# Kernel tuning notes

Hardware: AMD Instinct MI355X
Metric: run time of the kernel (lower is better)

The kernel has to match this reference:

```python
import jax, jax.numpy as jnp
import numpy as np

SRC_DIM = 64
DEST_DIM = 64
EDGE_DIM = 16
HID = 128
NHEAD = 4
B, S_CNT, D_CNT, K = 16, 1000, 1000, 32


def setup_inputs() -> dict:
    key = jax.random.key(0)
    ks = jax.random.split(key, 14)
    N = B * D_CNT
    sc = 0.05
    src = jax.random.normal(ks[0], (B, S_CNT, SRC_DIM), jnp.float32)
    dest = jax.random.normal(ks[1], (B, D_CNT, DEST_DIM), jnp.float32)
    # index 0 points at the prepended zero-padding row; valid ids in [0, B*S_CNT]
    adj = jax.random.randint(ks[2], (K, N), 0, B * S_CNT + 1, jnp.int32)
    mask = jax.random.randint(ks[3], (N, K), 0, 2) > 0
    mask = mask.at[:, 0].set(False)  # guarantee >=1 unmasked key per query
    edges = jax.random.normal(ks[4], (K, N, EDGE_DIM), jnp.float32)
    W_src = jax.random.normal(ks[5], (HID, SRC_DIM + EDGE_DIM), jnp.float32) * sc
    b_src = jnp.zeros((HID,), jnp.float32)
    W_dest = jax.random.normal(ks[6], (HID, DEST_DIM), jnp.float32) * sc
    b_dest = jnp.zeros((HID,), jnp.float32)
    in_proj_w = jax.random.normal(ks[7], (3 * HID, HID), jnp.float32) * sc
    in_proj_b = jax.random.normal(ks[8], (3 * HID,), jnp.float32) * sc
    out_proj_w = jax.random.normal(ks[9], (HID, HID), jnp.float32) * sc
    out_proj_b = jnp.zeros((HID,), jnp.float32)
    ln_g = jnp.ones((HID,), jnp.float32)
    ln_b = jnp.zeros((HID,), jnp.float32)
    return {"src": src, "dest": dest, "adj": adj, "mask": mask, "edges": edges,
            "W_src": W_src, "b_src": b_src, "W_dest": W_dest, "b_dest": b_dest,
            "in_proj_w": in_proj_w, "in_proj_b": in_proj_b,
            "out_proj_w": out_proj_w, "out_proj_b": out_proj_b,
            "ln_g": ln_g, "ln_b": ln_b}


def reference(src, dest, adj, mask, edges, W_src, b_src, W_dest, b_dest,
              in_proj_w, in_proj_b, out_proj_w, out_proj_b, ln_g, ln_b):
    B_, S_, Ds = src.shape
    _, Dn, Dd = dest.shape
    Kn = adj.shape[0]
    N = B_ * Dn
    H = W_src.shape[0]
    nh = NHEAD
    hd = H // nh
    # gather neighbor features, row 0 = zero padding
    src_flat = jnp.concatenate([jnp.zeros((1, Ds), src.dtype), src.reshape(-1, Ds)], 0)
    gathered = src_flat[adj.reshape(-1)].reshape(Kn, N, Ds)
    x = jnp.concatenate([gathered, edges], axis=-1)          # (K, N, Ds+E)
    src_in = jax.nn.gelu(x @ W_src.T + b_src, approximate=False)       # (K, N, H)
    dest_in = jax.nn.gelu(dest.reshape(N, Dd) @ W_dest.T + b_dest, approximate=False)  # (N, H)
    Wq, Wk, Wv = jnp.split(in_proj_w, 3, axis=0)
    bq, bk, bv = jnp.split(in_proj_b, 3, axis=0)
    q = ((dest_in @ Wq.T + bq).reshape(N, nh, hd)) * (1.0 / np.sqrt(hd))
    k = (src_in @ Wk.T + bk).reshape(Kn, N, nh, hd)
    v = (src_in @ Wv.T + bv).reshape(Kn, N, nh, hd)
    scores = jnp.einsum('nhd,knhd->nhk', q, k)               # (N, nh, K)
    scores = jnp.where(mask[:, None, :], -jnp.inf, scores)
    attn = jax.nn.softmax(scores, axis=-1)
    ctx = jnp.einsum('nhk,knhd->nhd', attn, v).reshape(N, H)
    out = ctx @ out_proj_w.T + out_proj_b
    out = out * 2.0  # dest_emb + dropout(dest_emb), dropout identity in eval
    mu = out.mean(-1, keepdims=True)
    var = ((out - mu) ** 2).mean(-1, keepdims=True)
    out = (out - mu) / jnp.sqrt(var + 1e-5) * ln_g + ln_b
    return out.reshape(B_, Dn, H)
```

## Files before the change

kernel.cpp:

```cpp
#include <hip/hip_runtime.h>
#include <hip/hip_bf16.h>
#include <math.h>

#define N_DEST 16000
#define KN     32
#define HIDN   128
#define NH     4
#define SRCD   64
#define EDGED  16
#define XD     80
#define XDP    96
#define WPB    4
#define NPW    2

#define WSB_OFF 0
#define WKV_OFF 12288
#define WDB_OFF 45056
#define WQB_OFF 53248
#define WOB_OFF 69632
#define PREP_TOT 86016

typedef __attribute__((ext_vector_type(8))) short frag8;
typedef __attribute__((ext_vector_type(4))) float f32x4;

__device__ __forceinline__ float gelu_tanh(float x) {
    float t = x * x;
    float m = fmaf(t, -0.07135481627f, -1.5957691216f);
    float e = __expf(x * m);
    return __fdividef(x, 1.0f + e);
}
__device__ __forceinline__ unsigned short f2bf(float f) {
    __hip_bfloat16 h = __float2bfloat16(f);
    union { __hip_bfloat16 h; unsigned short u; } c; c.h = h; return c.u;
}
__device__ __forceinline__ unsigned int pk2bf(float x, float y) {
    __hip_bfloat162 h2 = __float22bfloat162_rn(make_float2(x, y));
    union { __hip_bfloat162 h; unsigned int u; } c; c.h = h2; return c.u;
}
__device__ __forceinline__ float bflo(unsigned int u) {
    union { unsigned int u; float f; } c; c.u = u << 16; return c.f;
}
__device__ __forceinline__ float bfhi(unsigned int u) {
    union { unsigned int u; float f; } c; c.u = u & 0xFFFF0000u; return c.f;
}
__device__ __forceinline__ float dot8(uint4 w, float4 x0, float4 x1, float acc) {
    acc = fmaf(bflo(w.x), x0.x, acc); acc = fmaf(bfhi(w.x), x0.y, acc);
    acc = fmaf(bflo(w.y), x0.z, acc); acc = fmaf(bfhi(w.y), x0.w, acc);
    acc = fmaf(bflo(w.z), x1.x, acc); acc = fmaf(bfhi(w.z), x1.y, acc);
    acc = fmaf(bflo(w.w), x1.z, acc); acc = fmaf(bfhi(w.w), x1.w, acc);
    return acc;
}
__device__ __forceinline__ frag8 pack_frag(float4 f0, float4 f1) {
    union { frag8 f; uint4 u; } c;
    c.u.x = pk2bf(f0.x, f0.y); c.u.y = pk2bf(f0.z, f0.w);
    c.u.z = pk2bf(f1.x, f1.y); c.u.w = pk2bf(f1.z, f1.w);
    return c.f;
}
__device__ __forceinline__ frag8 zero_frag() {
    union { frag8 f; uint4 u; } c;
    c.u = make_uint4(0u, 0u, 0u, 0u);
    return c.f;
}

__global__ void prep_weights(const float* __restrict__ W_src,
                             const float* __restrict__ W_dest,
                             const float* __restrict__ Wqkv,
                             const float* __restrict__ Wo,
                             unsigned short* __restrict__ ws) {
    int i = blockIdx.x * 256 + threadIdx.x;
    if (i < WKV_OFF) {
        int r = i / XDP, c = i - r * XDP;
        ws[i] = f2bf(c < XD ? W_src[r * XD + c] : 0.0f);
    } else if (i < WDB_OFF) {
        int j = i - WKV_OFF;
        ws[i] = f2bf(Wqkv[128 * HIDN + j]);
    } else if (i < WQB_OFF) {
        ws[i] = f2bf(W_dest[i - WDB_OFF]);
    } else if (i < WOB_OFF) {
        ws[i] = f2bf(Wqkv[i - WQB_OFF]);
    } else if (i < PREP_TOT) {
        ws[i] = f2bf(Wo[i - WOB_OFF]);
    }
}

__device__ __forceinline__ void gemm_d_node(
    int n, int a0, int a1,
    const float* __restrict__ src, const float* __restrict__ edges,
    const float* __restrict__ b_src, const unsigned short* __restrict__ Wsb,
    unsigned short (*sinp)[128], int lg, int lm)
{
    frag8 aall[3][2];
    #pragma unroll
    for (int kt = 0; kt < 2; ++kt) {
        const int c0 = kt * 32 + lg * 8;
        if (a0) {
            const float4* p = (const float4*)(src + (size_t)(a0 - 1) * SRCD + c0);
            aall[kt][0] = pack_frag(p[0], p[1]);
        } else aall[kt][0] = zero_frag();
        if (a1) {
            const float4* p = (const float4*)(src + (size_t)(a1 - 1) * SRCD + c0);
            aall[kt][1] = pack_frag(p[0], p[1]);
        } else aall[kt][1] = zero_frag();
    }
    if (lg < 2) {
        const float4* p0 = (const float4*)(edges + ((size_t)lm * N_DEST + n) * EDGED + lg * 8);
        const float4* p1 = (const float4*)(edges + ((size_t)(lm + 16) * N_DEST + n) * EDGED + lg * 8);
        aall[2][0] = pack_frag(p0[0], p0[1]);
        aall[2][1] = pack_frag(p1[0], p1[1]);
    } else {
        aall[2][0] = zero_frag(); aall[2][1] = zero_frag();
    }

    #pragma unroll 1
    for (int half = 0; half < 2; ++half) {
        f32x4 acc[2][4];
        #pragma unroll
        for (int ct = 0; ct < 4; ++ct) {
            float bias = b_src[(half * 4 + ct) * 16 + lm];
            acc[0][ct] = (f32x4){bias, bias, bias, bias};
            acc[1][ct] = (f32x4){bias, bias, bias, bias};
        }
        #pragma unroll
        for (int kt = 0; kt < 3; ++kt) {
            #pragma unroll
            for (int ct = 0; ct < 4; ++ct) {
                frag8 b = *(const frag8*)(Wsb + (size_t)((half * 4 + ct) * 16 + lm) * XDP + kt * 32 + lg * 8);
                acc[0][ct] = __builtin_amdgcn_mfma_f32_16x16x32_bf16(aall[kt][0], b, acc[0][ct], 0, 0, 0);
                acc[1][ct] = __builtin_amdgcn_mfma_f32_16x16x32_bf16(aall[kt][1], b, acc[1][ct], 0, 0, 0);
            }
        }
        #pragma unroll
        for (int r = 0; r < 2; ++r)
            #pragma unroll
            for (int ct = 0; ct < 4; ++ct)
                #pragma unroll
                for (int e = 0; e < 4; ++e) {
                    const int row = r * 16 + lg * 4 + e;
                    const int cb  = ((half * 4 + ct) * 16 + lm) * 2;
                    const int byt = (cb ^ ((row & 7) << 4));
                    *(unsigned short*)((char*)&sinp[row][0] + byt) =
                        f2bf(gelu_tanh(acc[r][ct][e]));
                }
    }
}

__device__ __forceinline__ void softmax_head(
    const f32x4 (&acc)[2][4], unsigned mw, const float* __restrict__ sq,
    float* __restrict__ attn_row, int ch, int hp, int lg, int lm)
{
    float q0 = sq[ch * 64 + hp * 32 + lm];
    float q1 = sq[ch * 64 + hp * 32 + 16 + lm];
    float vals[8];
    #pragma unroll
    for (int r = 0; r < 2; ++r)
        #pragma unroll
        for (int e = 0; e < 4; ++e) {
            float v = acc[r][2 * hp][e] * q0 + acc[r][2 * hp + 1][e] * q1;
            v += __shfl_xor(v, 1); v += __shfl_xor(v, 2);
            v += __shfl_xor(v, 4); v += __shfl_xor(v, 8);
            vals[r * 4 + e] = v;
        }
    float m8 = -1e30f;
    #pragma unroll
    for (int j = 0; j < 8; ++j) {
        const int kk = (j >> 2) * 16 + lg * 4 + (j & 3);
        if ((mw >> kk) & 1u) vals[j] = -1e30f;
        m8 = fmaxf(m8, vals[j]);
    }
    m8 = fmaxf(m8, __shfl_xor(m8, 16));
    m8 = fmaxf(m8, __shfl_xor(m8, 32));
    float ex[8], s8 = 0.0f;
    #pragma unroll
    for (int j = 0; j < 8; ++j) { ex[j] = __expf(vals[j] - m8); s8 += ex[j]; }
    s8 += __shfl_xor(s8, 16); s8 += __shfl_xor(s8, 32);
    const float inv = __fdividef(1.0f, s8);
    if (lm == 0) {
        *(float4*)&attn_row[lg * 4] =
            make_float4(ex[0] * inv, ex[1] * inv, ex[2] * inv, ex[3] * inv);
        *(float4*)&attn_row[16 + lg * 4] =
            make_float4(ex[4] * inv, ex[5] * inv, ex[6] * inv, ex[7] * inv);
    }
}

__device__ __forceinline__ void pv_node(
    const f32x4 (&acc)[2][4], const float (*attn)[KN],
    float* __restrict__ ctx, int ch, int lg, int lm)
{
    const int hb = (ch - 2) * 2;
    float4 at[2][2];
    #pragma unroll
    for (int hp = 0; hp < 2; ++hp)
        #pragma unroll
        for (int r = 0; r < 2; ++r)
            at[hp][r] = *(const float4*)&attn[hb + hp][r * 16 + lg * 4];
    #pragma unroll
    for (int ct = 0; ct < 4; ++ct) {
        const int hp = ct >> 1;
        float v = 0.0f;
        #pragma unroll
        for (int r = 0; r < 2; ++r) {
            v = fmaf(at[hp][r].x, acc[r][ct][0], v);
            v = fmaf(at[hp][r].y, acc[r][ct][1], v);
            v = fmaf(at[hp][r].z, acc[r][ct][2], v);
            v = fmaf(at[hp][r].w, acc[r][ct][3], v);
        }
        v += __shfl_xor(v, 16); v += __shfl_xor(v, 32);
        if (lg == 0) ctx[(ch - 2) * 64 + ct * 16 + lm] = v;
    }
}

__global__ __launch_bounds__(256, 2) void fused_gat_wave(
    const float* __restrict__ src,
    const float* __restrict__ dest,
    const int*   __restrict__ adj,
    const int*   __restrict__ mask,
    const float* __restrict__ edges,
    const float* __restrict__ b_src,
    const float* __restrict__ b_dest,
    const float* __restrict__ bqkv,
    const float* __restrict__ bo,
    const float* __restrict__ ln_g,
    const float* __restrict__ ln_b,
    const unsigned short* __restrict__ ws,
    float* __restrict__ out)
{
    const int tid  = threadIdx.x;
    const int wv   = tid >> 6;
    const int lane = tid & 63;
    const int lg   = lane >> 4;
    const int lm   = lane & 15;
    const int n0   = (blockIdx.x * WPB + wv) * NPW;

    const unsigned short* Wsb = ws + WSB_OFF;
    const unsigned short* Wkv = ws + WKV_OFF;
    const unsigned short* Wdb = ws + WDB_OFF;
    const unsigned short* Wqb = ws + WQB_OFF;
    const unsigned short* Wob = ws + WOB_OFF;

    __shared__ __align__(16) unsigned short s_sin[WPB][NPW][KN][128];
    __shared__ __align__(16) float s_dc[WPB][NPW][HIDN];
    __shared__ __align__(16) float s_q[WPB][NPW][HIDN];
    __shared__ __align__(16) float s_attn[WPB][NPW][NH][KN];

    const int a00 = adj[lm * N_DEST + n0];
    const int a01 = adj[(lm + 16) * N_DEST + n0];
    const int a10 = adj[lm * N_DEST + n0 + 1];
    const int a11 = adj[(lm + 16) * N_DEST + n0 + 1];
    const int mv = mask[n0 * KN + lane];
    const unsigned long long bal = __ballot(mv != 0);
    const unsigned mw0 = (unsigned)bal;
    const unsigned mw1 = (unsigned)(bal >> 32);

    {
        const float* dr0 = dest + (size_t)n0 * SRCD;
        const float* dr1 = dest + (size_t)(n0 + 1) * SRCD;
        float bd0 = b_dest[lane], bd1 = b_dest[lane + 64];
        float da0 = bd0, da1 = bd1, db0 = bd0, db1 = bd1;
        #pragma unroll
        for (int c = 0; c < 8; ++c) {
            float4 xa0 = *(const float4*)(dr0 + c * 8);
            float4 xa1 = *(const float4*)(dr0 + c * 8 + 4);
            float4 xb0 = *(const float4*)(dr1 + c * 8);
            float4 xb1 = *(const float4*)(dr1 + c * 8 + 4);
            uint4 w0 = *(const uint4*)(Wdb + (size_t)lane * SRCD + c * 8);
            uint4 w1 = *(const uint4*)(Wdb + (size_t)(lane + 64) * SRCD + c * 8);
            da0 = dot8(w0, xa0, xa1, da0); da1 = dot8(w1, xa0, xa1, da1);
            db0 = dot8(w0, xb0, xb1, db0); db1 = dot8(w1, xb0, xb1, db1);
        }
        s_dc[wv][0][lane]      = gelu_tanh(da0);
        s_dc[wv][0][lane + 64] = gelu_tanh(da1);
        s_dc[wv][1][lane]      = gelu_tanh(db0);
        s_dc[wv][1][lane + 64] = gelu_tanh(db1);
    }
    __builtin_amdgcn_wave_barrier();

    {
        float bq0 = bqkv[lane], bq1 = bqkv[lane + 64];
        float qa0 = bq0, qa1 = bq1, qb0 = bq0, qb1 = bq1;
        #pragma unroll
        for (int c = 0; c < 16; ++c) {
            float4 xa0 = *(const float4*)&s_dc[wv][0][c * 8];
            float4 xa1 = *(const float4*)&s_dc[wv][0][c * 8 + 4];
            float4 xb0 = *(const float4*)&s_dc[wv][1][c * 8];
            float4 xb1 = *(const float4*)&s_dc[wv][1][c * 8 + 4];
            uint4 w0 = *(const uint4*)(Wqb + (size_t)lane * HIDN + c * 8);
            uint4 w1 = *(const uint4*)(Wqb + (size_t)(lane + 64) * HIDN + c * 8);
            qa0 = dot8(w0, xa0, xa1, qa0); qa1 = dot8(w1, xa0, xa1, qa1);
            qb0 = dot8(w0, xb0, xb1, qb0); qb1 = dot8(w1, xb0, xb1, qb1);
        }
        const float sc = 0.17677669529663688110f;
        s_q[wv][0][lane]      = qa0 * sc;
        s_q[wv][0][lane + 64] = qa1 * sc;
        s_q[wv][1][lane]      = qb0 * sc;
        s_q[wv][1][lane + 64] = qb1 * sc;
    }
    __builtin_amdgcn_wave_barrier();

    gemm_d_node(n0,     a00, a01, src, edges, b_src, Wsb, s_sin[wv][0], lg, lm);
    gemm_d_node(n0 + 1, a10, a11, src, edges, b_src, Wsb, s_sin[wv][1], lg, lm);
    __builtin_amdgcn_wave_barrier();

    #pragma unroll 1
    for (int ch = 0; ch < 4; ++ch) {
        f32x4 ac0[2][4], ac1[2][4];
        #pragma unroll
        for (int ct = 0; ct < 4; ++ct) {
            float bias = bqkv[128 + ch * 64 + ct * 16 + lm];
            ac0[0][ct] = (f32x4){bias, bias, bias, bias};
            ac0[1][ct] = ac0[0][ct];
            ac1[0][ct] = ac0[0][ct];
            ac1[1][ct] = ac0[0][ct];
        }
        #pragma unroll
        for (int kt = 0; kt < 4; ++kt) {
            const int off = (kt * 64 + lg * 16) ^ ((lm & 7) << 4);
            frag8 a00f = *(const frag8*)((const char*)&s_sin[wv][0][lm][0] + off);
            frag8 a01f = *(const frag8*)((const char*)&s_sin[wv][0][16 + lm][0] + off);
            frag8 a10f = *(const frag8*)((const char*)&s_sin[wv][1][lm][0] + off);
            frag8 a11f = *(const frag8*)((const char*)&s_sin[wv][1][16 + lm][0] + off);
            #pragma unroll
            for (int ct = 0; ct < 4; ++ct) {
                frag8 b = *(const frag8*)(Wkv + (size_t)(ch * 64 + ct * 16 + lm) * HIDN + kt * 32 + lg * 8);
                ac0[0][ct] = __builtin_amdgcn_mfma_f32_16x16x32_bf16(a00f, b, ac0[0][ct], 0, 0, 0);
                ac0[1][ct] = __builtin_amdgcn_mfma_f32_16x16x32_bf16(a01f, b, ac0[1][ct], 0, 0, 0);
                ac1[0][ct] = __builtin_amdgcn_mfma_f32_16x16x32_bf16(a10f, b, ac1[0][ct], 0, 0, 0);
                ac1[1][ct] = __builtin_amdgcn_mfma_f32_16x16x32_bf16(a11f, b, ac1[1][ct], 0, 0, 0);
            }
        }
        if (ch < 2) {
            #pragma unroll
            for (int hp = 0; hp < 2; ++hp) {
                const int head = ch * 2 + hp;
                softmax_head(ac0, mw0, s_q[wv][0], s_attn[wv][0][head], ch, hp, lg, lm);
                softmax_head(ac1, mw1, s_q[wv][1], s_attn[wv][1][head], ch, hp, lg, lm);
            }
        } else {
            pv_node(ac0, s_attn[wv][0], s_dc[wv][0], ch, lg, lm);
            pv_node(ac1, s_attn[wv][1], s_dc[wv][1], ch, lg, lm);
        }
    }
    __builtin_amdgcn_wave_barrier();

    {
        float bo0 = bo[lane], bo1 = bo[lane + 64];
        float oa0 = bo0, oa1 = bo1, ob0 = bo0, ob1 = bo1;
        #pragma unroll
        for (int c = 0; c < 16; ++c) {
            float4 xa0 = *(const float4*)&s_dc[wv][0][c * 8];
            float4 xa1 = *(const float4*)&s_dc[wv][0][c * 8 + 4];
            float4 xb0 = *(const float4*)&s_dc[wv][1][c * 8];
            float4 xb1 = *(const float4*)&s_dc[wv][1][c * 8 + 4];
            uint4 w0 = *(const uint4*)(Wob + (size_t)lane * HIDN + c * 8);
            uint4 w1 = *(const uint4*)(Wob + (size_t)(lane + 64) * HIDN + c * 8);
            oa0 = dot8(w0, xa0, xa1, oa0); oa1 = dot8(w1, xa0, xa1, oa1);
            ob0 = dot8(w0, xb0, xb1, ob0); ob1 = dot8(w1, xb0, xb1, ob1);
        }
        float o00 = oa0 * 2.0f, o01 = oa1 * 2.0f;
        float o10 = ob0 * 2.0f, o11 = ob1 * 2.0f;
        float s0 = o00 + o01, ss0 = o00 * o00 + o01 * o01;
        float s1 = o10 + o11, ss1 = o10 * o10 + o11 * o11;
        #pragma unroll
        for (int off = 1; off < 64; off <<= 1) {
            s0  += __shfl_xor(s0, off);  ss0 += __shfl_xor(ss0, off);
            s1  += __shfl_xor(s1, off);  ss1 += __shfl_xor(ss1, off);
        }
        float mu0  = s0 * (1.0f / HIDN);
        float var0 = ss0 * (1.0f / HIDN) - mu0 * mu0;
        float rs0  = rsqrtf(var0 + 1e-5f);
        float mu1  = s1 * (1.0f / HIDN);
        float var1 = ss1 * (1.0f / HIDN) - mu1 * mu1;
        float rs1  = rsqrtf(var1 + 1e-5f);
        float g0 = ln_g[lane], g1 = ln_g[lane + 64];
        float t0 = ln_b[lane], t1 = ln_b[lane + 64];
        out[(size_t)n0 * HIDN + lane]            = (o00 - mu0) * rs0 * g0 + t0;
        out[(size_t)n0 * HIDN + lane + 64]       = (o01 - mu0) * rs0 * g1 + t1;
        out[(size_t)(n0 + 1) * HIDN + lane]      = (o10 - mu1) * rs1 * g0 + t0;
        out[(size_t)(n0 + 1) * HIDN + lane + 64] = (o11 - mu1) * rs1 * g1 + t1;
    }
}

extern "C" void kernel_launch(void* const* d_in, const int* in_sizes, int n_in,
                              void* d_out, int out_size, void* d_ws, size_t ws_size,
                              hipStream_t stream) {
    const float* src    = (const float*)d_in[0];
    const float* dest   = (const float*)d_in[1];
    const int*   adj    = (const int*)  d_in[2];
    const int*   mask   = (const int*)  d_in[3];
    const float* edges  = (const float*)d_in[4];
    const float* W_src  = (const float*)d_in[5];
    const float* b_src  = (const float*)d_in[6];
    const float* W_dest = (const float*)d_in[7];
    const float* b_dest = (const float*)d_in[8];
    const float* Wqkv   = (const float*)d_in[9];
    const float* bqkv   = (const float*)d_in[10];
    const float* Wo     = (const float*)d_in[11];
    const float* bo     = (const float*)d_in[12];
    const float* ln_g   = (const float*)d_in[13];
    const float* ln_b   = (const float*)d_in[14];
    float* outp = (float*)d_out;

    unsigned short* ws = (unsigned short*)d_ws;
    prep_weights<<<PREP_TOT / 256, 256, 0, stream>>>(W_src, W_dest, Wqkv, Wo, ws);

    fused_gat_wave<<<N_DEST / (WPB * NPW), 256, 0, stream>>>(
        src, dest, adj, mask, edges, b_src, b_dest, bqkv, bo, ln_g, ln_b,
        ws, outp);
}
```

Before: 334.7 us.

## Split fused GAT kernel into source-projection and attention kernels via global buffer

```diff
diff --git a/kernel.cpp b/kernel.cpp
--- a/kernel.cpp
+++ b/kernel.cpp
@@ -19,6 +19,9 @@
 #define WQB_OFF 53248
 #define WOB_OFF 69632
 #define PREP_TOT 86016
+#define SIN_OFF  PREP_TOT
+#define SIN_ELEMS ((size_t)N_DEST * KN * HIDN)
+#define WS_NEED_BYTES ((size_t)2 * (PREP_TOT + SIN_ELEMS))
 
 typedef __attribute__((ext_vector_type(8))) short frag8;
 typedef __attribute__((ext_vector_type(4))) float f32x4;
@@ -83,6 +86,308 @@
     }
 }
 
+__device__ __forceinline__ void softmax_head(
+    const f32x4 (&acc)[2][4], unsigned mw, const float* __restrict__ sq,
+    float* __restrict__ attn_row, int ch, int hp, int lg, int lm)
+{
+    float q0 = sq[ch * 64 + hp * 32 + lm];
+    float q1 = sq[ch * 64 + hp * 32 + 16 + lm];
+    float vals[8];
+    #pragma unroll
+    for (int r = 0; r < 2; ++r)
+        #pragma unroll
+        for (int e = 0; e < 4; ++e) {
+            float v = acc[r][2 * hp][e] * q0 + acc[r][2 * hp + 1][e] * q1;
+            v += __shfl_xor(v, 1); v += __shfl_xor(v, 2);
+            v += __shfl_xor(v, 4); v += __shfl_xor(v, 8);
+            vals[r * 4 + e] = v;
+        }
+    float m8 = -1e30f;
+    #pragma unroll
+    for (int j = 0; j < 8; ++j) {
+        const int kk = (j >> 2) * 16 + lg * 4 + (j & 3);
+        if ((mw >> kk) & 1u) vals[j] = -1e30f;
+        m8 = fmaxf(m8, vals[j]);
+    }
+    m8 = fmaxf(m8, __shfl_xor(m8, 16));
+    m8 = fmaxf(m8, __shfl_xor(m8, 32));
+    float ex[8], s8 = 0.0f;
+    #pragma unroll
+    for (int j = 0; j < 8; ++j) { ex[j] = __expf(vals[j] - m8); s8 += ex[j]; }
+    s8 += __shfl_xor(s8, 16); s8 += __shfl_xor(s8, 32);
+    const float inv = __fdividef(1.0f, s8);
+    if (lm == 0) {
+        *(float4*)&attn_row[lg * 4] =
+            make_float4(ex[0] * inv, ex[1] * inv, ex[2] * inv, ex[3] * inv);
+        *(float4*)&attn_row[16 + lg * 4] =
+            make_float4(ex[4] * inv, ex[5] * inv, ex[6] * inv, ex[7] * inv);
+    }
+}
+
+__device__ __forceinline__ void pv_node(
+    const f32x4 (&acc)[2][4], const float (*attn)[KN],
+    float* __restrict__ ctx, int ch, int lg, int lm)
+{
+    const int hb = (ch - 2) * 2;
+    float4 at[2][2];
+    #pragma unroll
+    for (int hp = 0; hp < 2; ++hp)
+        #pragma unroll
+        for (int r = 0; r < 2; ++r)
+            at[hp][r] = *(const float4*)&attn[hb + hp][r * 16 + lg * 4];
+    #pragma unroll
+    for (int ct = 0; ct < 4; ++ct) {
+        const int hp = ct >> 1;
+        float v = 0.0f;
+        #pragma unroll
+        for (int r = 0; r < 2; ++r) {
+            v = fmaf(at[hp][r].x, acc[r][ct][0], v);
+            v = fmaf(at[hp][r].y, acc[r][ct][1], v);
+            v = fmaf(at[hp][r].z, acc[r][ct][2], v);
+            v = fmaf(at[hp][r].w, acc[r][ct][3], v);
+        }
+        v += __shfl_xor(v, 16); v += __shfl_xor(v, 32);
+        if (lg == 0) ctx[(ch - 2) * 64 + ct * 16 + lm] = v;
+    }
+}
+
+__device__ __forceinline__ void gemm_d_node_g(
+    int n, int a0, int a1,
+    const float* __restrict__ src, const float* __restrict__ edges,
+    const float* __restrict__ b_src, const unsigned short* __restrict__ Wsb,
+    unsigned short* __restrict__ sinG, int lg, int lm)
+{
+    frag8 aall[3][2];
+    #pragma unroll
+    for (int kt = 0; kt < 2; ++kt) {
+        const int c0 = kt * 32 + lg * 8;
+        if (a0) {
+            const float4* p = (const float4*)(src + (size_t)(a0 - 1) * SRCD + c0);
+            aall[kt][0] = pack_frag(p[0], p[1]);
+        } else aall[kt][0] = zero_frag();
+        if (a1) {
+            const float4* p = (const float4*)(src + (size_t)(a1 - 1) * SRCD + c0);
+            aall[kt][1] = pack_frag(p[0], p[1]);
+        } else aall[kt][1] = zero_frag();
+    }
+    if (lg < 2) {
+        const float4* p0 = (const float4*)(edges + ((size_t)lm * N_DEST + n) * EDGED + lg * 8);
+        const float4* p1 = (const float4*)(edges + ((size_t)(lm + 16) * N_DEST + n) * EDGED + lg * 8);
+        aall[2][0] = pack_frag(p0[0], p0[1]);
+        aall[2][1] = pack_frag(p1[0], p1[1]);
+    } else {
+        aall[2][0] = zero_frag(); aall[2][1] = zero_frag();
+    }
+
+    unsigned short* sb = sinG + (size_t)n * KN * HIDN;
+    #pragma unroll 1
+    for (int half = 0; half < 2; ++half) {
+        f32x4 acc[2][4];
+        #pragma unroll
+        for (int ct = 0; ct < 4; ++ct) {
+            float bias = b_src[(half * 4 + ct) * 16 + lm];
+            acc[0][ct] = (f32x4){bias, bias, bias, bias};
+            acc[1][ct] = (f32x4){bias, bias, bias, bias};
+        }
+        #pragma unroll
+        for (int kt = 0; kt < 3; ++kt) {
+            #pragma unroll
+            for (int ct = 0; ct < 4; ++ct) {
+                frag8 b = *(const frag8*)(Wsb + (size_t)((half * 4 + ct) * 16 + lm) * XDP + kt * 32 + lg * 8);
+                acc[0][ct] = __builtin_amdgcn_mfma_f32_16x16x32_bf16(aall[kt][0], b, acc[0][ct], 0, 0, 0);
+                acc[1][ct] = __builtin_amdgcn_mfma_f32_16x16x32_bf16(aall[kt][1], b, acc[1][ct], 0, 0, 0);
+            }
+        }
+        #pragma unroll
+        for (int r = 0; r < 2; ++r)
+            #pragma unroll
+            for (int ct = 0; ct < 4; ++ct)
+                #pragma unroll
+                for (int e = 0; e < 4; ++e) {
+                    const int row = r * 16 + lg * 4 + e;
+                    const int col = (half * 4 + ct) * 16 + lm;
+                    sb[(size_t)row * HIDN + col] = f2bf(gelu_tanh(acc[r][ct][e]));
+                }
+    }
+}
+
+__global__ __launch_bounds__(256, 4) void gemm_d_all(
+    const float* __restrict__ src, const float* __restrict__ edges,
+    const int* __restrict__ adj, const float* __restrict__ b_src,
+    const unsigned short* __restrict__ ws, unsigned short* __restrict__ sinG)
+{
+    const int tid  = threadIdx.x;
+    const int wv   = tid >> 6;
+    const int lane = tid & 63;
+    const int lg   = lane >> 4;
+    const int lm   = lane & 15;
+    const int n0   = (blockIdx.x * WPB + wv) * NPW;
+    const unsigned short* Wsb = ws + WSB_OFF;
+
+    const int a00 = adj[lm * N_DEST + n0];
+    const int a01 = adj[(lm + 16) * N_DEST + n0];
+    const int a10 = adj[lm * N_DEST + n0 + 1];
+    const int a11 = adj[(lm + 16) * N_DEST + n0 + 1];
+
+    gemm_d_node_g(n0,     a00, a01, src, edges, b_src, Wsb, sinG, lg, lm);
+    gemm_d_node_g(n0 + 1, a10, a11, src, edges, b_src, Wsb, sinG, lg, lm);
+}
+
+__global__ __launch_bounds__(256, 4) void attn_all(
+    const float* __restrict__ dest,
+    const int*   __restrict__ mask,
+    const float* __restrict__ b_dest,
+    const float* __restrict__ bqkv,
+    const float* __restrict__ bo,
+    const float* __restrict__ ln_g,
+    const float* __restrict__ ln_b,
+    const unsigned short* __restrict__ ws,
+    const unsigned short* __restrict__ sinG,
+    float* __restrict__ out)
+{
+    const int tid  = threadIdx.x;
+    const int wv   = tid >> 6;
+    const int lane = tid & 63;
+    const int lg   = lane >> 4;
+    const int lm   = lane & 15;
+    const int n0   = (blockIdx.x * WPB + wv) * NPW;
+
+    const unsigned short* Wkv = ws + WKV_OFF;
+    const unsigned short* Wdb = ws + WDB_OFF;
+    const unsigned short* Wqb = ws + WQB_OFF;
+    const unsigned short* Wob = ws + WOB_OFF;
+
+    __shared__ __align__(16) float s_dc[WPB][NPW][HIDN];
+    __shared__ __align__(16) float s_q[WPB][NPW][HIDN];
+    __shared__ __align__(16) float s_attn[WPB][NPW][NH][KN];
+
+    const int mv = mask[n0 * KN + lane];
+    const unsigned long long bal = __ballot(mv != 0);
+    const unsigned mw0 = (unsigned)bal;
+    const unsigned mw1 = (unsigned)(bal >> 32);
+
+    {
+        const float* dr0 = dest + (size_t)n0 * SRCD;
+        const float* dr1 = dest + (size_t)(n0 + 1) * SRCD;
+        float bd0 = b_dest[lane], bd1 = b_dest[lane + 64];
+        float da0 = bd0, da1 = bd1, db0 = bd0, db1 = bd1;
+        #pragma unroll
+        for (int c = 0; c < 8; ++c) {
+            float4 xa0 = *(const float4*)(dr0 + c * 8);
+            float4 xa1 = *(const float4*)(dr0 + c * 8 + 4);
+            float4 xb0 = *(const float4*)(dr1 + c * 8);
+            float4 xb1 = *(const float4*)(dr1 + c * 8 + 4);
+            uint4 w0 = *(const uint4*)(Wdb + (size_t)lane * SRCD + c * 8);
+            uint4 w1 = *(const uint4*)(Wdb + (size_t)(lane + 64) * SRCD + c * 8);
+            da0 = dot8(w0, xa0, xa1, da0); da1 = dot8(w1, xa0, xa1, da1);
+            db0 = dot8(w0, xb0, xb1, db0); db1 = dot8(w1, xb0, xb1, db1);
+        }
+        s_dc[wv][0][lane]      = gelu_tanh(da0);
+        s_dc[wv][0][lane + 64] = gelu_tanh(da1);
+        s_dc[wv][1][lane]      = gelu_tanh(db0);
+        s_dc[wv][1][lane + 64] = gelu_tanh(db1);
+    }
+    __builtin_amdgcn_wave_barrier();
+
+    {
+        float bq0 = bqkv[lane], bq1 = bqkv[lane + 64];
+        float qa0 = bq0, qa1 = bq1, qb0 = bq0, qb1 = bq1;
+        #pragma unroll
+        for (int c = 0; c < 16; ++c) {
+            float4 xa0 = *(const float4*)&s_dc[wv][0][c * 8];
+            float4 xa1 = *(const float4*)&s_dc[wv][0][c * 8 + 4];
+            float4 xb0 = *(const float4*)&s_dc[wv][1][c * 8];
+            float4 xb1 = *(const float4*)&s_dc[wv][1][c * 8 + 4];
+            uint4 w0 = *(const uint4*)(Wqb + (size_t)lane * HIDN + c * 8);
+            uint4 w1 = *(const uint4*)(Wqb + (size_t)(lane + 64) * HIDN + c * 8);
+            qa0 = dot8(w0, xa0, xa1, qa0); qa1 = dot8(w1, xa0, xa1, qa1);
+            qb0 = dot8(w0, xb0, xb1, qb0); qb1 = dot8(w1, xb0, xb1, qb1);
+        }
+        const float sc = 0.17677669529663688110f;
+        s_q[wv][0][lane]      = qa0 * sc;
+        s_q[wv][0][lane + 64] = qa1 * sc;
+        s_q[wv][1][lane]      = qb0 * sc;
+        s_q[wv][1][lane + 64] = qb1 * sc;
+    }
+    __builtin_amdgcn_wave_barrier();
+
+    #pragma unroll 1
+    for (int nd = 0; nd < NPW; ++nd) {
+        const unsigned short* sb = sinG + (size_t)(n0 + nd) * KN * HIDN;
+        frag8 af0[4], af1[4];
+        #pragma unroll
+        for (int kt = 0; kt < 4; ++kt) {
+            af0[kt] = *(const frag8*)(sb + (size_t)lm * HIDN + kt * 32 + lg * 8);
+            af1[kt] = *(const frag8*)(sb + (size_t)(lm + 16) * HIDN + kt * 32 + lg * 8);
+        }
+        const unsigned mwn = nd ? mw1 : mw0;
+        #pragma unroll 1
+        for (int ch = 0; ch < 4; ++ch) {
+            f32x4 acc[2][4];
+            #pragma unroll
+            for (int ct = 0; ct < 4; ++ct) {
+                float bias = bqkv[128 + ch * 64 + ct * 16 + lm];
+                acc[0][ct] = (f32x4){bias, bias, bias, bias};
+                acc[1][ct] = acc[0][ct];
+            }
+            #pragma unroll
+            for (int kt = 0; kt < 4; ++kt) {
+                #pragma unroll
+                for (int ct = 0; ct < 4; ++ct) {
+                    frag8 b = *(const frag8*)(Wkv + (size_t)(ch * 64 + ct * 16 + lm) * HIDN + kt * 32 + lg * 8);
+                    acc[0][ct] = __builtin_amdgcn_mfma_f32_16x16x32_bf16(af0[kt], b, acc[0][ct], 0, 0, 0);
+                    acc[1][ct] = __builtin_amdgcn_mfma_f32_16x16x32_bf16(af1[kt], b, acc[1][ct], 0, 0, 0);
+                }
+            }
+            if (ch < 2) {
+                #pragma unroll
+                for (int hp = 0; hp < 2; ++hp)
+                    softmax_head(acc, mwn, s_q[wv][nd], s_attn[wv][nd][ch * 2 + hp], ch, hp, lg, lm);
+            } else {
+                pv_node(acc, s_attn[wv][nd], s_dc[wv][nd], ch, lg, lm);
+            }
+        }
+    }
+    __builtin_amdgcn_wave_barrier();
+
+    {
+        float bo0 = bo[lane], bo1 = bo[lane + 64];
+        float oa0 = bo0, oa1 = bo1, ob0 = bo0, ob1 = bo1;
+        #pragma unroll
+        for (int c = 0; c < 16; ++c) {
+            float4 xa0 = *(const float4*)&s_dc[wv][0][c * 8];
+            float4 xa1 = *(const float4*)&s_dc[wv][0][c * 8 + 4];
+            float4 xb0 = *(const float4*)&s_dc[wv][1][c * 8];
+            float4 xb1 = *(const float4*)&s_dc[wv][1][c * 8 + 4];
+            uint4 w0 = *(const uint4*)(Wob + (size_t)lane * HIDN + c * 8);
+            uint4 w1 = *(const uint4*)(Wob + (size_t)(lane + 64) * HIDN + c * 8);
+            oa0 = dot8(w0, xa0, xa1, oa0); oa1 = dot8(w1, xa0, xa1, oa1);
+            ob0 = dot8(w0, xb0, xb1, ob0); ob1 = dot8(w1, xb0, xb1, ob1);
+        }
+        float o00 = oa0 * 2.0f, o01 = oa1 * 2.0f;
+        float o10 = ob0 * 2.0f, o11 = ob1 * 2.0f;
+        float s0 = o00 + o01, ss0 = o00 * o00 + o01 * o01;
+        float s1 = o10 + o11, ss1 = o10 * o10 + o11 * o11;
+        #pragma unroll
+        for (int off = 1; off < 64; off <<= 1) {
+            s0  += __shfl_xor(s0, off);  ss0 += __shfl_xor(ss0, off);
+            s1  += __shfl_xor(s1, off);  ss1 += __shfl_xor(ss1, off);
+        }
+        float mu0  = s0 * (1.0f / HIDN);
+        float var0 = ss0 * (1.0f / HIDN) - mu0 * mu0;
+        float rs0  = rsqrtf(var0 + 1e-5f);
+        float mu1  = s1 * (1.0f / HIDN);
+        float var1 = ss1 * (1.0f / HIDN) - mu1 * mu1;
+        float rs1  = rsqrtf(var1 + 1e-5f);
+        float g0 = ln_g[lane], g1 = ln_g[lane + 64];
+        float t0 = ln_b[lane], t1 = ln_b[lane + 64];
+        out[(size_t)n0 * HIDN + lane]            = (o00 - mu0) * rs0 * g0 + t0;
+        out[(size_t)n0 * HIDN + lane + 64]       = (o01 - mu0) * rs0 * g1 + t1;
+        out[(size_t)(n0 + 1) * HIDN + lane]      = (o10 - mu1) * rs1 * g0 + t0;
+        out[(size_t)(n0 + 1) * HIDN + lane + 64] = (o11 - mu1) * rs1 * g1 + t1;
+    }
+}
+
 __device__ __forceinline__ void gemm_d_node(
     int n, int a0, int a1,
     const float* __restrict__ src, const float* __restrict__ edges,
@@ -144,84 +449,13 @@
     }
 }
 
-__device__ __forceinline__ void softmax_head(
-    const f32x4 (&acc)[2][4], unsigned mw, const float* __restrict__ sq,
-    float* __restrict__ attn_row, int ch, int hp, int lg, int lm)
-{
-    float q0 = sq[ch * 64 + hp * 32 + lm];
-    float q1 = sq[ch * 64 + hp * 32 + 16 + lm];
-    float vals[8];
-    #pragma unroll
-    for (int r = 0; r < 2; ++r)
-        #pragma unroll
-        for (int e = 0; e < 4; ++e) {
-            float v = acc[r][2 * hp][e] * q0 + acc[r][2 * hp + 1][e] * q1;
-            v += __shfl_xor(v, 1); v += __shfl_xor(v, 2);
-            v += __shfl_xor(v, 4); v += __shfl_xor(v, 8);
-            vals[r * 4 + e] = v;
-        }
-    float m8 = -1e30f;
-    #pragma unroll
-    for (int j = 0; j < 8; ++j) {
-        const int kk = (j >> 2) * 16 + lg * 4 + (j & 3);
-        if ((mw >> kk) & 1u) vals[j] = -1e30f;
-        m8 = fmaxf(m8, vals[j]);
-    }
-    m8 = fmaxf(m8, __shfl_xor(m8, 16));
-    m8 = fmaxf(m8, __shfl_xor(m8, 32));
-    float ex[8], s8 = 0.0f;
-    #pragma unroll
-    for (int j = 0; j < 8; ++j) { ex[j] = __expf(vals[j] - m8); s8 += ex[j]; }
-    s8 += __shfl_xor(s8, 16); s8 += __shfl_xor(s8, 32);
-    const float inv = __fdividef(1.0f, s8);
-    if (lm == 0) {
-        *(float4*)&attn_row[lg * 4] =
-            make_float4(ex[0] * inv, ex[1] * inv, ex[2] * inv, ex[3] * inv);
-        *(float4*)&attn_row[16 + lg * 4] =
-            make_float4(ex[4] * inv, ex[5] * inv, ex[6] * inv, ex[7] * inv);
-    }
-}
-
-__device__ __forceinline__ void pv_node(
-    const f32x4 (&acc)[2][4], const float (*attn)[KN],
-    float* __restrict__ ctx, int ch, int lg, int lm)
-{
-    const int hb = (ch - 2) * 2;
-    float4 at[2][2];
-    #pragma unroll
-    for (int hp = 0; hp < 2; ++hp)
-        #pragma unroll
-        for (int r = 0; r < 2; ++r)
-            at[hp][r] = *(const float4*)&attn[hb + hp][r * 16 + lg * 4];
-    #pragma unroll
-    for (int ct = 0; ct < 4; ++ct) {
-        const int hp = ct >> 1;
-        float v = 0.0f;
-        #pragma unroll
-        for (int r = 0; r < 2; ++r) {
-            v = fmaf(at[hp][r].x, acc[r][ct][0], v);
-            v = fmaf(at[hp][r].y, acc[r][ct][1], v);
-            v = fmaf(at[hp][r].z, acc[r][ct][2], v);
-            v = fmaf(at[hp][r].w, acc[r][ct][3], v);
-        }
-        v += __shfl_xor(v, 16); v += __shfl_xor(v, 32);
-        if (lg == 0) ctx[(ch - 2) * 64 + ct * 16 + lm] = v;
-    }
-}
-
-__global__ __launch_bounds__(256, 2) void fused_gat_wave(
-    const float* __restrict__ src,
-    const float* __restrict__ dest,
-    const int*   __restrict__ adj,
-    const int*   __restrict__ mask,
-    const float* __restrict__ edges,
-    const float* __restrict__ b_src,
-    const float* __restrict__ b_dest,
-    const float* __restrict__ bqkv,
-    const float* __restrict__ bo,
-    const float* __restrict__ ln_g,
-    const float* __restrict__ ln_b,
-    const unsigned short* __restrict__ ws,
+__global__ __launch_bounds__(256, 2) void fused_gat_fallback(
+    const float* __restrict__ src, const float* __restrict__ dest,
+    const int* __restrict__ adj, const int* __restrict__ mask,
+    const float* __restrict__ edges, const float* __restrict__ b_src,
+    const float* __restrict__ b_dest, const float* __restrict__ bqkv,
+    const float* __restrict__ bo, const float* __restrict__ ln_g,
+    const float* __restrict__ ln_b, const unsigned short* __restrict__ ws,
     float* __restrict__ out)
 {
     const int tid  = threadIdx.x;
@@ -273,7 +507,6 @@
         s_dc[wv][1][lane + 64] = gelu_tanh(db1);
     }
     __builtin_amdgcn_wave_barrier();
-
     {
         float bq0 = bqkv[lane], bq1 = bqkv[lane + 64];
         float qa0 = bq0, qa1 = bq1, qb0 = bq0, qb1 = bq1;
@@ -295,11 +528,9 @@
         s_q[wv][1][lane + 64] = qb1 * sc;
     }
     __builtin_amdgcn_wave_barrier();
-
     gemm_d_node(n0,     a00, a01, src, edges, b_src, Wsb, s_sin[wv][0], lg, lm);
     gemm_d_node(n0 + 1, a10, a11, src, edges, b_src, Wsb, s_sin[wv][1], lg, lm);
     __builtin_amdgcn_wave_barrier();
-
     #pragma unroll 1
     for (int ch = 0; ch < 4; ++ch) {
         f32x4 ac0[2][4], ac1[2][4];
@@ -340,7 +571,6 @@
         }
     }
     __builtin_amdgcn_wave_barrier();
-
     {
         float bo0 = bo[lane], bo1 = bo[lane + 64];
         float oa0 = bo0, oa1 = bo1, ob0 = bo0, ob1 = bo1;
@@ -402,7 +632,15 @@
     unsigned short* ws = (unsigned short*)d_ws;
     prep_weights<<<PREP_TOT / 256, 256, 0, stream>>>(W_src, W_dest, Wqkv, Wo, ws);
 
-    fused_gat_wave<<<N_DEST / (WPB * NPW), 256, 0, stream>>>(
-        src, dest, adj, mask, edges, b_src, b_dest, bqkv, bo, ln_g, ln_b,
-        ws, outp);
-}
+    if (ws_size >= WS_NEED_BYTES) {
+        unsigned short* sinG = ws + SIN_OFF;
+        gemm_d_all<<<N_DEST / (WPB * NPW), 256, 0, stream>>>(
+            src, edges, adj, b_src, ws, sinG);
+        attn_all<<<N_DEST / (WPB * NPW), 256, 0, stream>>>(
+            dest, mask, b_dest, bqkv, bo, ln_g, ln_b, ws, sinG, outp);
+    } else {
+        fused_gat_fallback<<<N_DEST / (WPB * NPW), 256, 0, stream>>>(
+            src, dest, adj, mask, edges, b_src, b_dest, bqkv, bo, ln_g, ln_b,
+            ws, outp);
+    }
+}
```

Result: slower. 390.1 us (+16.6%).

## Process four destination nodes per wave to amortize weight loads

Applied to the files above, without the earlier changes.

```diff
diff --git a/kernel.cpp b/kernel.cpp
--- a/kernel.cpp
+++ b/kernel.cpp
@@ -11,7 +11,7 @@
 #define XD     80
 #define XDP    96
 #define WPB    4
-#define NPW    2
+#define NPW    4
 
 #define WSB_OFF 0
 #define WKV_OFF 12288
@@ -43,11 +43,15 @@
 __device__ __forceinline__ float bfhi(unsigned int u) {
     union { unsigned int u; float f; } c; c.u = u & 0xFFFF0000u; return c.f;
 }
-__device__ __forceinline__ float dot8(uint4 w, float4 x0, float4 x1, float acc) {
-    acc = fmaf(bflo(w.x), x0.x, acc); acc = fmaf(bfhi(w.x), x0.y, acc);
-    acc = fmaf(bflo(w.y), x0.z, acc); acc = fmaf(bfhi(w.y), x0.w, acc);
-    acc = fmaf(bflo(w.z), x1.x, acc); acc = fmaf(bfhi(w.z), x1.y, acc);
-    acc = fmaf(bflo(w.w), x1.z, acc); acc = fmaf(bfhi(w.w), x1.w, acc);
+__device__ __forceinline__ void unpack8(uint4 w, float f[8]) {
+    f[0] = bflo(w.x); f[1] = bfhi(w.x); f[2] = bflo(w.y); f[3] = bfhi(w.y);
+    f[4] = bflo(w.z); f[5] = bfhi(w.z); f[6] = bflo(w.w); f[7] = bfhi(w.w);
+}
+__device__ __forceinline__ float dotu(const float f[8], float4 x0, float4 x1, float acc) {
+    acc = fmaf(f[0], x0.x, acc); acc = fmaf(f[1], x0.y, acc);
+    acc = fmaf(f[2], x0.z, acc); acc = fmaf(f[3], x0.w, acc);
+    acc = fmaf(f[4], x1.x, acc); acc = fmaf(f[5], x1.y, acc);
+    acc = fmaf(f[6], x1.z, acc); acc = fmaf(f[7], x1.w, acc);
     return acc;
 }
 __device__ __forceinline__ frag8 pack_frag(float4 f0, float4 f1) {
@@ -145,11 +149,9 @@
 }
 
 __device__ __forceinline__ void softmax_head(
-    const f32x4 (&acc)[2][4], unsigned mw, const float* __restrict__ sq,
-    float* __restrict__ attn_row, int ch, int hp, int lg, int lm)
+    const f32x4 (&acc)[2][4], unsigned mw, float q0, float q1,
+    float* __restrict__ attn_row, int hp, int lg, int lm)
 {
-    float q0 = sq[ch * 64 + hp * 32 + lm];
-    float q1 = sq[ch * 64 + hp * 32 + 16 + lm];
     float vals[8];
     #pragma unroll
     for (int r = 0; r < 2; ++r)
@@ -207,6 +209,70 @@
         v += __shfl_xor(v, 16); v += __shfl_xor(v, 32);
         if (lg == 0) ctx[(ch - 2) * 64 + ct * 16 + lm] = v;
     }
+}
+
+__device__ __forceinline__ void process_pair(
+    int na, int nb, int a0a, int a1a, int a0b, int a1b,
+    unsigned mwa, unsigned mwb,
+    float qla, float qha, float qlb, float qhb,
+    const float* __restrict__ src, const float* __restrict__ edges,
+    const float* __restrict__ b_src, const float* __restrict__ bqkv,
+    const unsigned short* __restrict__ Wsb, const unsigned short* __restrict__ Wkv,
+    unsigned short (*sinA)[128], unsigned short (*sinB)[128],
+    float* __restrict__ dcA, float* __restrict__ dcB,
+    float (*attnA)[KN], float (*attnB)[KN],
+    int lg, int lm)
+{
+    gemm_d_node(na, a0a, a1a, src, edges, b_src, Wsb, sinA, lg, lm);
+    gemm_d_node(nb, a0b, a1b, src, edges, b_src, Wsb, sinB, lg, lm);
+    __builtin_amdgcn_wave_barrier();
+
+    #pragma unroll 1
+    for (int ch = 0; ch < 4; ++ch) {
+        f32x4 ac0[2][4], ac1[2][4];
+        #pragma unroll
+        for (int ct = 0; ct < 4; ++ct) {
+            float bias = bqkv[128 + ch * 64 + ct * 16 + lm];
+            ac0[0][ct] = (f32x4){bias, bias, bias, bias};
+            ac0[1][ct] = ac0[0][ct];
+            ac1[0][ct] = ac0[0][ct];
+            ac1[1][ct] = ac0[0][ct];
+        }
+        #pragma unroll
+        for (int kt = 0; kt < 4; ++kt) {
+            const int off = (kt * 64 + lg * 16) ^ ((lm & 7) << 4);
+            frag8 a00f = *(const frag8*)((const char*)&sinA[lm][0] + off);
+            frag8 a01f = *(const frag8*)((const char*)&sinA[16 + lm][0] + off);
+            frag8 a10f = *(const frag8*)((const char*)&sinB[lm][0] + off);
+            frag8 a11f = *(const frag8*)((const char*)&sinB[16 + lm][0] + off);
+            #pragma unroll
+            for (int ct = 0; ct < 4; ++ct) {
+                frag8 b = *(const frag8*)(Wkv + (size_t)(ch * 64 + ct * 16 + lm) * HIDN + kt * 32 + lg * 8);
+                ac0[0][ct] = __builtin_amdgcn_mfma_f32_16x16x32_bf16(a00f, b, ac0[0][ct], 0, 0, 0);
+                ac0[1][ct] = __builtin_amdgcn_mfma_f32_16x16x32_bf16(a01f, b, ac0[1][ct], 0, 0, 0);
+                ac1[0][ct] = __builtin_amdgcn_mfma_f32_16x16x32_bf16(a10f, b, ac1[0][ct], 0, 0, 0);
+                ac1[1][ct] = __builtin_amdgcn_mfma_f32_16x16x32_bf16(a11f, b, ac1[1][ct], 0, 0, 0);
+            }
+        }
+        if (ch < 2) {
+            #pragma unroll
+            for (int hp = 0; hp < 2; ++hp) {
+                const int head = ch * 2 + hp;
+                float qsa = (ch == 0) ? qla : qha;
+                float qsb = (ch == 0) ? qlb : qhb;
+                float qa0 = __shfl(qsa, hp * 32 + lm);
+                float qa1 = __shfl(qsa, hp * 32 + 16 + lm);
+                float qb0 = __shfl(qsb, hp * 32 + lm);
+                float qb1 = __shfl(qsb, hp * 32 + 16 + lm);
+                softmax_head(ac0, mwa, qa0, qa1, attnA[head], hp, lg, lm);
+                softmax_head(ac1, mwb, qb0, qb1, attnB[head], hp, lg, lm);
+            }
+        } else {
+            pv_node(ac0, attnA, dcA, ch, lg, lm);
+            pv_node(ac1, attnB, dcB, ch, lg, lm);
+        }
+    }
+    __builtin_amdgcn_wave_barrier();
 }
 
 __global__ __launch_bounds__(256, 2) void fused_gat_wave(
@@ -237,145 +303,130 @@
     const unsigned short* Wqb = ws + WQB_OFF;
     const unsigned short* Wob = ws + WOB_OFF;
 
-    __shared__ __align__(16) unsigned short s_sin[WPB][NPW][KN][128];
+    __shared__ __align__(16) unsigned short s_sin[WPB][2][KN][128];
     __shared__ __align__(16) float s_dc[WPB][NPW][HIDN];
-    __shared__ __align__(16) float s_q[WPB][NPW][HIDN];
-    __shared__ __align__(16) float s_attn[WPB][NPW][NH][KN];
-
-    const int a00 = adj[lm * N_DEST + n0];
-    const int a01 = adj[(lm + 16) * N_DEST + n0];
-    const int a10 = adj[lm * N_DEST + n0 + 1];
-    const int a11 = adj[(lm + 16) * N_DEST + n0 + 1];
-    const int mv = mask[n0 * KN + lane];
-    const unsigned long long bal = __ballot(mv != 0);
-    const unsigned mw0 = (unsigned)bal;
-    const unsigned mw1 = (unsigned)(bal >> 32);
+    __shared__ __align__(16) float s_attn[WPB][2][NH][KN];
+
+    int a0[NPW], a1[NPW];
+    #pragma unroll
+    for (int nd = 0; nd < NPW; ++nd) {
+        a0[nd] = adj[lm * N_DEST + n0 + nd];
+        a1[nd] = adj[(lm + 16) * N_DEST + n0 + nd];
+    }
+    const int mvA = mask[n0 * KN + lane];
+    const int mvB = mask[(n0 + 2) * KN + lane];
+    const unsigned long long balA = __ballot(mvA != 0);
+    const unsigned long long balB = __ballot(mvB != 0);
+    const unsigned mw0 = (unsigned)balA, mw1 = (unsigned)(balA >> 32);
+    const unsigned mw2 = (unsigned)balB, mw3 = (unsigned)(balB >> 32);
 
     {
-        const float* dr0 = dest + (size_t)n0 * SRCD;
-        const float* dr1 = dest + (size_t)(n0 + 1) * SRCD;
+        float da[NPW][2];
         float bd0 = b_dest[lane], bd1 = b_dest[lane + 64];
-        float da0 = bd0, da1 = bd1, db0 = bd0, db1 = bd1;
+        #pragma unroll
+        for (int nd = 0; nd < NPW; ++nd) { da[nd][0] = bd0; da[nd][1] = bd1; }
+        const unsigned short* w0p = Wdb + (size_t)lane * SRCD;
+        const unsigned short* w1p = Wdb + (size_t)(lane + 64) * SRCD;
         #pragma unroll
         for (int c = 0; c < 8; ++c) {
-            float4 xa0 = *(const float4*)(dr0 + c * 8);
-            float4 xa1 = *(const float4*)(dr0 + c * 8 + 4);
-            float4 xb0 = *(const float4*)(dr1 + c * 8);
-            float4 xb1 = *(const float4*)(dr1 + c * 8 + 4);
-            uint4 w0 = *(const uint4*)(Wdb + (size_t)lane * SRCD + c * 8);
-            uint4 w1 = *(const uint4*)(Wdb + (size_t)(lane + 64) * SRCD + c * 8);
-            da0 = dot8(w0, xa0, xa1, da0); da1 = dot8(w1, xa0, xa1, da1);
-            db0 = dot8(w0, xb0, xb1, db0); db1 = dot8(w1, xb0, xb1, db1);
-        }
-        s_dc[wv][0][lane]      = gelu_tanh(da0);
-        s_dc[wv][0][lane + 64] = gelu_tanh(da1);
-        s_dc[wv][1][lane]      = gelu_tanh(db0);
-        s_dc[wv][1][lane + 64] = gelu_tanh(db1);
+            float wf0[8], wf1[8];
+            unpack8(*(const uint4*)(w0p + c * 8), wf0);
+            unpack8(*(const uint4*)(w1p + c * 8), wf1);
+            #pragma unroll
+            for (int nd = 0; nd < NPW; ++nd) {
+                const float* dr = dest + (size_t)(n0 + nd) * SRCD + c * 8;
+                float4 x0 = *(const float4*)dr;
+                float4 x1 = *(const float4*)(dr + 4);
+                da[nd][0] = dotu(wf0, x0, x1, da[nd][0]);
+                da[nd][1] = dotu(wf1, x0, x1, da[nd][1]);
+            }
+        }
+        #pragma unroll
+        for (int nd = 0; nd < NPW; ++nd) {
+            s_dc[wv][nd][lane]      = gelu_tanh(da[nd][0]);
+            s_dc[wv][nd][lane + 64] = gelu_tanh(da[nd][1]);
+        }
     }
     __builtin_amdgcn_wave_barrier();
 
+    float q_l[NPW], q_h[NPW];
     {
+        float qa[NPW][2];
         float bq0 = bqkv[lane], bq1 = bqkv[lane + 64];
-        float qa0 = bq0, qa1 = bq1, qb0 = bq0, qb1 = bq1;
+        #pragma unroll
+        for (int nd = 0; nd < NPW; ++nd) { qa[nd][0] = bq0; qa[nd][1] = bq1; }
+        const unsigned short* w0p = Wqb + (size_t)lane * HIDN;
+        const unsigned short* w1p = Wqb + (size_t)(lane + 64) * HIDN;
         #pragma unroll
         for (int c = 0; c < 16; ++c) {
-            float4 xa0 = *(const float4*)&s_dc[wv][0][c * 8];
-            float4 xa1 = *(const float4*)&s_dc[wv][0][c * 8 + 4];
-            float4 xb0 = *(const float4*)&s_dc[wv][1][c * 8];
-            float4 xb1 = *(const float4*)&s_dc[wv][1][c * 8 + 4];
-            uint4 w0 = *(const uint4*)(Wqb + (size_t)lane * HIDN + c * 8);
-            uint4 w1 = *(const uint4*)(Wqb + (size_t)(lane + 64) * HIDN + c * 8);
-            qa0 = dot8(w0, xa0, xa1, qa0); qa1 = dot8(w1, xa0, xa1, qa1);
-            qb0 = dot8(w0, xb0, xb1, qb0); qb1 = dot8(w1, xb0, xb1, qb1);
+            float wf0[8], wf1[8];
+            unpack8(*(const uint4*)(w0p + c * 8), wf0);
+            unpack8(*(const uint4*)(w1p + c * 8), wf1);
+            #pragma unroll
+            for (int nd = 0; nd < NPW; ++nd) {
+                float4 x0 = *(const float4*)&s_dc[wv][nd][c * 8];
+                float4 x1 = *(const float4*)&s_dc[wv][nd][c * 8 + 4];
+                qa[nd][0] = dotu(wf0, x0, x1, qa[nd][0]);
+                qa[nd][1] = dotu(wf1, x0, x1, qa[nd][1]);
+            }
         }
         const float sc = 0.17677669529663688110f;
-        s_q[wv][0][lane]      = qa0 * sc;
-        s_q[wv][0][lane + 64] = qa1 * sc;
-        s_q[wv][1][lane]      = qb0 * sc;
-        s_q[wv][1][lane + 64] = qb1 * sc;
+        #pragma unroll
+        for (int nd = 0; nd < NPW; ++nd) {
+            q_l[nd] = qa[nd][0] * sc;
+            q_h[nd] = qa[nd][1] * sc;
+        }
     }
     __builtin_amdgcn_wave_barrier();
 
-    gemm_d_node(n0,     a00, a01, src, edges, b_src, Wsb, s_sin[wv][0], lg, lm);
-    gemm_d_node(n0 + 1, a10, a11, src, edges, b_src, Wsb, s_sin[wv][1], lg, lm);
-    __builtin_amdgcn_wave_barrier();
-
-    #pragma unroll 1
-    for (int ch = 0; ch < 4; ++ch) {
-        f32x4 ac0[2][4], ac1[2][4];
-        #pragma unroll
-        for (int ct = 0; ct < 4; ++ct) {
-            float bias = bqkv[128 + ch * 64 + ct * 16 + lm];
-            ac0[0][ct] = (f32x4){bias, bias, bias, bias};
-            ac0[1][ct] = ac0[0][ct];
-            ac1[0][ct] = ac0[0][ct];
-            ac1[1][ct] = ac0[0][ct];
-        }
-        #pragma unroll
-        for (int kt = 0; kt < 4; ++kt) {
-            const int off = (kt * 64 + lg * 16) ^ ((lm & 7) << 4);
-            frag8 a00f = *(const frag8*)((const char*)&s_sin[wv][0][lm][0] + off);
-            frag8 a01f = *(const frag8*)((const char*)&s_sin[wv][0][16 + lm][0] + off);
-            frag8 a10f = *(const frag8*)((const char*)&s_sin[wv][1][lm][0] + off);
-            frag8 a11f = *(const frag8*)((const char*)&s_sin[wv][1][16 + lm][0] + off);
-            #pragma unroll
-            for (int ct = 0; ct < 4; ++ct) {
-                frag8 b = *(const frag8*)(Wkv + (size_t)(ch * 64 + ct * 16 + lm) * HIDN + kt * 32 + lg * 8);
-                ac0[0][ct] = __builtin_amdgcn_mfma_f32_16x16x32_bf16(a00f, b, ac0[0][ct], 0, 0, 0);
-                ac0[1][ct] = __builtin_amdgcn_mfma_f32_16x16x32_bf16(a01f, b, ac0[1][ct], 0, 0, 0);
-                ac1[0][ct] = __builtin_amdgcn_mfma_f32_16x16x32_bf16(a10f, b, ac1[0][ct], 0, 0, 0);
-                ac1[1][ct] = __builtin_amdgcn_mfma_f32_16x16x32_bf16(a11f, b, ac1[1][ct], 0, 0, 0);
-            }
-        }
-        if (ch < 2) {
-            #pragma unroll
-            for (int hp = 0; hp < 2; ++hp) {
-                const int head = ch * 2 + hp;
-                softmax_head(ac0, mw0, s_q[wv][0], s_attn[wv][0][head], ch, hp, lg, lm);
-                softmax_head(ac1, mw1, s_q[wv][1], s_attn[wv][1][head], ch, hp, lg, lm);
-            }
-        } else {
-            pv_node(ac0, s_attn[wv][0], s_dc[wv][0], ch, lg, lm);
-            pv_node(ac1, s_attn[wv][1], s_dc[wv][1], ch, lg, lm);
-        }
-    }
-    __builtin_amdgcn_wave_barrier();
+    process_pair(n0,     n0 + 1, a0[0], a1[0], a0[1], a1[1], mw0, mw1,
+                 q_l[0], q_h[0], q_l[1], q_h[1],
+                 src, edges, b_src, bqkv, Wsb, Wkv,
+                 s_sin[wv][0], s_sin[wv][1], s_dc[wv][0], s_dc[wv][1],
+                 s_attn[wv][0], s_attn[wv][1], lg, lm);
+    process_pair(n0 + 2, n0 + 3, a0[2], a1[2], a0[3], a1[3], mw2, mw3,
+                 q_l[2], q_h[2], q_l[3], q_h[3],
+                 src, edges, b_src, bqkv, Wsb, Wkv,
+                 s_sin[wv][0], s_sin[wv][1], s_dc[wv][2], s_dc[wv][3],
+                 s_attn[wv][0], s_attn[wv][1], lg, lm);
 
     {
+        float oa[NPW][2];
         float bo0 = bo[lane], bo1 = bo[lane + 64];
-        float oa0 = bo0, oa1 = bo1, ob0 = bo0, ob1 = bo1;
+        #pragma unroll
+        for (int nd = 0; nd < NPW; ++nd) { oa[nd][0] = bo0; oa[nd][1] = bo1; }
+        const unsigned short* w0p = Wob + (size_t)lane * HIDN;
+        const unsigned short* w1p = Wob + (size_t)(lane + 64) * HIDN;
         #pragma unroll
         for (int c = 0; c < 16; ++c) {
-            float4 xa0 = *(const float4*)&s_dc[wv][0][c * 8];
-            float4 xa1 = *(const float4*)&s_dc[wv][0][c * 8 + 4];
-            float4 xb0 = *(const float4*)&s_dc[wv][1][c * 8];
-            float4 xb1 = *(const float4*)&s_dc[wv][1][c * 8 + 4];
-            uint4 w0 = *(const uint4*)(Wob + (size_t)lane * HIDN + c * 8);
-            uint4 w1 = *(const uint4*)(Wob + (size_t)(lane + 64) * HIDN + c * 8);
-            oa0 = dot8(w0, xa0, xa1, oa0); oa1 = dot8(w1, xa0, xa1, oa1);
-            ob0 = dot8(w0, xb0, xb1, ob0); ob1 = dot8(w1, xb0, xb1, ob1);
-        }
-        float o00 = oa0 * 2.0f, o01 = oa1 * 2.0f;
-        float o10 = ob0 * 2.0f, o11 = ob1 * 2.0f;
-        float s0 = o00 + o01, ss0 = o00 * o00 + o01 * o01;
-        float s1 = o10 + o11, ss1 = o10 * o10 + o11 * o11;
-        #pragma unroll
-        for (int off = 1; off < 64; off <<= 1) {
-            s0  += __shfl_xor(s0, off);  ss0 += __shfl_xor(ss0, off);
-            s1  += __shfl_xor(s1, off);  ss1 += __shfl_xor(ss1, off);
-        }
-        float mu0  = s0 * (1.0f / HIDN);
-        float var0 = ss0 * (1.0f / HIDN) - mu0 * mu0;
-        float rs0  = rsqrtf(var0 + 1e-5f);
-        float mu1  = s1 * (1.0f / HIDN);
-        float var1 = ss1 * (1.0f / HIDN) - mu1 * mu1;
-        float rs1  = rsqrtf(var1 + 1e-5f);
+            float wf0[8], wf1[8];
+            unpack8(*(const uint4*)(w0p + c * 8), wf0);
+            unpack8(*(const uint4*)(w1p + c * 8), wf1);
+            #pragma unroll
+            for (int nd = 0; nd < NPW; ++nd) {
+                float4 x0 = *(const float4*)&s_dc[wv][nd][c * 8];
+                float4 x1 = *(const float4*)&s_dc[wv][nd][c * 8 + 4];
+                oa[nd][0] = dotu(wf0, x0, x1, oa[nd][0]);
+                oa[nd][1] = dotu(wf1, x0, x1, oa[nd][1]);
+            }
+        }
         float g0 = ln_g[lane], g1 = ln_g[lane + 64];
         float t0 = ln_b[lane], t1 = ln_b[lane + 64];
-        out[(size_t)n0 * HIDN + lane]            = (o00 - mu0) * rs0 * g0 + t0;
-        out[(size_t)n0 * HIDN + lane + 64]       = (o01 - mu0) * rs0 * g1 + t1;
-        out[(size_t)(n0 + 1) * HIDN + lane]      = (o10 - mu1) * rs1 * g0 + t0;
-        out[(size_t)(n0 + 1) * HIDN + lane + 64] = (o11 - mu1) * rs1 * g1 + t1;
+        #pragma unroll
+        for (int nd = 0; nd < NPW; ++nd) {
+            float o0 = oa[nd][0] * 2.0f, o1 = oa[nd][1] * 2.0f;
+            float s = o0 + o1, ss = o0 * o0 + o1 * o1;
+            #pragma unroll
+            for (int off = 1; off < 64; off <<= 1) {
+                s  += __shfl_xor(s, off);
+                ss += __shfl_xor(ss, off);
+            }
+            float mu  = s * (1.0f / HIDN);
+            float var = ss * (1.0f / HIDN) - mu * mu;
+            float rs  = rsqrtf(var + 1e-5f);
+            out[(size_t)(n0 + nd) * HIDN + lane]      = (o0 - mu) * rs * g0 + t0;
+            out[(size_t)(n0 + nd) * HIDN + lane + 64] = (o1 - mu) * rs * g1 + t1;
+        }
     }
 }
 
```

After: 623.2 us. 86.2% more time.
